# Kernel optimization log

Hardware: AMD Instinct MI355X
Metric: run time of the kernel (lower is better)

## Reference

```python
import jax, jax.numpy as jnp
import numpy as np

S = 20  # number of standard amino acids; hardcoded in the original layer


def expm_fixed(A, squarings=6, terms=14):
    """Scaling-and-squaring matrix exponential with fixed squaring count.
    A: (..., n, n). tau*Q entries are small (tau ~ softplus(-3)), so a fixed
    2^-6 scaling + Taylor-14 matches tf.linalg.expm to fp32 tolerance."""
    A = A / (2.0 ** squarings)
    I = jnp.broadcast_to(jnp.eye(A.shape[-1], dtype=A.dtype), A.shape)
    out = I
    term = I
    for i in range(1, terms + 1):
        term = jnp.matmul(term, A) / i
        out = out + term
    for _ in range(squarings):
        out = jnp.matmul(out, out)
    return out


def make_rate_matrix(R, p, eps=1e-16):
    """R: (N, s, s) symmetric exchangeabilities, zero diag. p: (N, s) equilibrium."""
    Q = R * p[:, None, :]                       # Q[i,j] = R[i,j] * p[j]
    diag = jnp.sum(Q, axis=-1, keepdims=True)   # (N, s, 1)
    eye = jnp.eye(Q.shape[-1], dtype=Q.dtype)
    Q = Q - diag * eye
    mue = jnp.sum(p[:, :, None] * diag, axis=-2, keepdims=True)  # (N,1,1)
    return Q / jnp.maximum(mue, eps)


def setup_inputs() -> dict:
    key = jax.random.key(0)
    ks = jax.random.split(key, 6)
    m, b, L, k, nr = 2, 256, 1024, 4, 100
    inputs = jax.random.uniform(ks[0], (m, b, L, S), dtype=jnp.float32)
    rate_indices = jax.random.randint(ks[1], (m, b), 0, nr, dtype=jnp.int64)
    # rate_init = constant(-3.0); small jitter so gradients are non-degenerate
    tau_kernel = -3.0 + 0.1 * jax.random.normal(ks[2], (m, nr), dtype=jnp.float32)
    exchangeability_kernel = 0.1 * jax.random.normal(ks[3], (m, k, S, S), dtype=jnp.float32)
    equilibrium_kernel = 0.1 * jax.random.normal(ks[4], (m, k, S), dtype=jnp.float32)
    per_matrix_rates_kernel = 0.1 * jax.random.normal(ks[5], (m, k), dtype=jnp.float32)
    return {
        "inputs": inputs,
        "tau_kernel": tau_kernel,
        "exchangeability_kernel": exchangeability_kernel,
        "equilibrium_kernel": equilibrium_kernel,
        "per_matrix_rates_kernel": per_matrix_rates_kernel,
        "rate_indices": rate_indices,
    }


def reference(inputs, tau_kernel, exchangeability_kernel, equilibrium_kernel,
              per_matrix_rates_kernel, rate_indices):
    m, b, L, s = inputs.shape
    k = exchangeability_kernel.shape[1]
    # make_tau(subset): gather per-sequence times then softplus
    tau = jax.nn.softplus(jnp.take_along_axis(tau_kernel, rate_indices, axis=1))  # (m,b)
    # per-matrix rates
    pmr = jax.nn.softplus(per_matrix_rates_kernel)  # (m,k)
    mut_rates = tau[:, :, None] * pmr[:, None, :]   # (m,b,k)
    # make_R: symmetrize, softplus, zero diagonal
    K = exchangeability_kernel
    R = jax.nn.softplus(0.5 * (K + jnp.swapaxes(K, -1, -2)))
    R = R * (1.0 - jnp.eye(s, dtype=R.dtype))       # (m,k,s,s)
    # make_p
    p = jax.nn.softmax(equilibrium_kernel, axis=-1)  # (m,k,s)
    # normalized rate matrices
    Q = make_rate_matrix(R.reshape(-1, s, s), p.reshape(-1, s)).reshape(m, k, s, s)
    # tau * Q, batched over sequences: (m,b,k,s,s)
    tauQ = mut_rates[..., None, None] * Q[:, None]
    P = expm_fixed(tauQ.reshape(-1, s, s)).reshape(m, b, k, s, s)
    # vector-format inputs path (non-transposed): mbLz,mbkzs->mbLks
    anc = jnp.einsum('mblz,mbkzs->mblks', inputs, P)
    # documented output: (num_model, b, L, num_matrices*s)
    return anc.reshape(m, b, L, k * s)
```

## Files before the change

kernel.cpp:

```cpp
#include <hip/hip_runtime.h>
#include <math.h>

#define M_  2
#define B_  256
#define L_  1024
#define K_  4
#define S_  20
#define NR_ 100
#define NTERM 7

typedef float f32x4_t __attribute__((ext_vector_type(4)));

__device__ __forceinline__ float softplusf(float x) {
    return x > 20.0f ? x : log1pf(expf(x));
}

__global__ __launch_bounds__(512)
void qpow_kernel(const float* __restrict__ exch,
                 const float* __restrict__ equil,
                 float*       __restrict__ Qpow)
{
    __shared__ float sQ[400];
    __shared__ float sT[2][400];
    __shared__ float sRow[20];

    const int blk = blockIdx.x;
    const int kk = blk % K_;
    const int mm = blk / K_;
    const int tid = threadIdx.x;
    const bool act = tid < 400;
    const int i = tid / 20;
    const int j = tid - i * 20;

    float p[20];
    float Q0 = 0.0f, rowsum = 0.0f;

    if (act) {
        const float* eq = equil + (mm * K_ + kk) * S_;
        float mx = eq[0];
        #pragma unroll
        for (int z = 1; z < 20; ++z) mx = fmaxf(mx, eq[z]);
        float s = 0.0f;
        #pragma unroll
        for (int z = 0; z < 20; ++z) { p[z] = expf(eq[z] - mx); s += p[z]; }
        const float inv = 1.0f / s;
        #pragma unroll
        for (int z = 0; z < 20; ++z) p[z] *= inv;

        const float* Kx = exch + (mm * K_ + kk) * S_ * S_;
        float R = (i == j) ? 0.0f : softplusf(0.5f * (Kx[i * 20 + j] + Kx[j * 20 + i]));
        Q0 = R * p[j];
        sQ[tid] = Q0;
    }
    __syncthreads();

    if (act) {
        rowsum = 0.0f;
        #pragma unroll
        for (int z = 0; z < 20; ++z) rowsum += sQ[i * 20 + z];
        if (j == 0) sRow[i] = rowsum;
    }
    __syncthreads();

    float* Tout = Qpow + (size_t)blk * (NTERM * 400);
    if (act) {
        float mue = 0.0f;
        #pragma unroll
        for (int z = 0; z < 20; ++z) mue += p[z] * sRow[z];
        float q = (Q0 - ((i == j) ? rowsum : 0.0f)) / fmaxf(mue, 1e-16f);
        sQ[tid] = q;
        sT[0][tid] = q;
        Tout[tid] = q;
    }
    __syncthreads();

    int cur = 0;
    for (int n = 2; n <= NTERM; ++n) {
        if (act) {
            float acc = 0.0f;
            #pragma unroll
            for (int z = 0; z < 20; ++z) acc += sT[cur][i * 20 + z] * sQ[z * 20 + j];
            acc /= (float)n;
            sT[cur ^ 1][tid] = acc;
            Tout[(n - 1) * 400 + tid] = acc;
        }
        __syncthreads();
        cur ^= 1;
    }
}

__global__ __launch_bounds__(512)
void pbuild_kernel(const float* __restrict__ Qpow,
                   const float* __restrict__ tauk,
                   const float* __restrict__ pmrk,
                   float*       __restrict__ Pws)
{
    const int blk = blockIdx.x;
    const int kk = blk % K_;
    const int rr = (blk / K_) % NR_;
    const int mm = blk / (K_ * NR_);
    const int tid = threadIdx.x;
    if (tid >= 400) return;

    const float mu = softplusf(tauk[mm * NR_ + rr]) * softplusf(pmrk[mm * K_ + kk]);
    const float* T = Qpow + ((size_t)(mm * K_ + kk) * NTERM) * 400 + tid;

    float acc = (tid % 21 == 0) ? 1.0f : 0.0f;
    float mp = mu;
    #pragma unroll
    for (int n = 0; n < NTERM; ++n) { acc = fmaf(mp, T[n * 400], acc); mp *= mu; }
    Pws[(size_t)blk * 400 + tid] = acc;
}

#define SPANR 256
#define TPB3  320

__device__ __forceinline__ void fma4(float4& a, float s, const float4& p) {
    a.x = fmaf(s, p.x, a.x);
    a.y = fmaf(s, p.y, a.y);
    a.z = fmaf(s, p.z, a.z);
    a.w = fmaf(s, p.w, a.w);
}

__device__ __forceinline__ void nt_store4(float* dst, const float4& v) {
    f32x4_t w;
    w.x = v.x; w.y = v.y; w.z = v.z; w.w = v.w;
    __builtin_nontemporal_store(w, (f32x4_t*)dst);
}

__global__ __launch_bounds__(TPB3)
void einsum_kernel(const float* __restrict__ inp,
                   const float* __restrict__ Pws,
                   const int*   __restrict__ ridx,
                   float*       __restrict__ out)
{
    __shared__ float Pl[K_ * 400];
    __shared__ float inL[SPANR * 20];

    const int bx      = blockIdx.x;
    const int quarter = bx & 3;
    const int mb      = bx >> 2;
    const int mm      = mb >> 8;
    const int tid     = threadIdx.x;
    const int t       = tid % 20;
    const int rg      = tid / 20;
    const int k       = t / 5;
    const int s0      = (t % 5) * 4;

    const int r = ridx[mb];

    {
        const float4* Psrc = (const float4*)(Pws + ((size_t)(mm * NR_ + r) * K_) * 400);
        float4* Pd = (float4*)Pl;
        Pd[tid] = Psrc[tid];
        if (tid < 80) Pd[320 + tid] = Psrc[320 + tid];

        const size_t row0g = (size_t)mb * L_ + (size_t)quarter * SPANR;
        const float4* Isrc = (const float4*)(inp + row0g * 20);
        float4* Id = (float4*)inL;
        #pragma unroll
        for (int q = 0; q < 4; ++q) Id[tid + q * TPB3] = Isrc[tid + q * TPB3];
    }
    __syncthreads();

    const size_t row0 = (size_t)mb * L_ + (size_t)quarter * SPANR;
    float* ob = out + row0 * 80 + k * 20 + s0;
    const float* Pk = Pl + k * 400 + s0;

    float4 acc[16];
    #pragma unroll
    for (int rr = 0; rr < 16; ++rr) acc[rr] = make_float4(0.f, 0.f, 0.f, 0.f);

    #pragma unroll
    for (int z4 = 0; z4 < 5; ++z4) {
        const float4 p0 = *(const float4*)(Pk + (z4 * 4 + 0) * 20);
        const float4 p1 = *(const float4*)(Pk + (z4 * 4 + 1) * 20);
        const float4 p2 = *(const float4*)(Pk + (z4 * 4 + 2) * 20);
        const float4 p3 = *(const float4*)(Pk + (z4 * 4 + 3) * 20);
        #pragma unroll
        for (int rr = 0; rr < 16; ++rr) {
            const int l = rg + rr * 16;
            const float4 av = *(const float4*)(inL + l * 20 + z4 * 4);
            fma4(acc[rr], av.x, p0);
            fma4(acc[rr], av.y, p1);
            fma4(acc[rr], av.z, p2);
            fma4(acc[rr], av.w, p3);
        }
    }

    #pragma unroll
    for (int rr = 0; rr < 16; ++rr) {
        const int l = rg + rr * 16;
        nt_store4(ob + (size_t)l * 80, acc[rr]);
    }
}

extern "C" void kernel_launch(void* const* d_in, const int* in_sizes, int n_in,
                              void* d_out, int out_size, void* d_ws, size_t ws_size,
                              hipStream_t stream) {
    const float* inp   = (const float*)d_in[0];
    const float* tauk  = (const float*)d_in[1];
    const float* exch  = (const float*)d_in[2];
    const float* equil = (const float*)d_in[3];
    const float* pmrk  = (const float*)d_in[4];
    const int*   ridx  = (const int*)d_in[5];
    float* outp = (float*)d_out;

    float* Qpow = (float*)d_ws;
    float* Pws  = Qpow + (size_t)M_ * K_ * NTERM * 400;

    qpow_kernel<<<M_ * K_, 512, 0, stream>>>(exch, equil, Qpow);
    pbuild_kernel<<<M_ * NR_ * K_, 512, 0, stream>>>(Qpow, tauk, pmrk, Pws);
    einsum_kernel<<<M_ * B_ * (L_ / SPANR), TPB3, 0, stream>>>(inp, Pws, ridx, outp);
}
```

Before: 57.69 us.

## Fuse Q-power and P-build kernels; use plain stores in einsum

Merges the Taylor-term kernel and the per-rate P builder into one kernel. Each thread keeps its seven Q-power terms in registers and loops over all 100 rates to write P directly, which removes one launch and the workspace round trip. The trade-off is that the P build now runs on only 8 blocks instead of 800, so this stage loses parallelism. The einsum output also switches from nontemporal stores to ordinary float4 stores.

```diff
diff --git a/kernel.cpp b/kernel.cpp
--- a/kernel.cpp
+++ b/kernel.cpp
@@ -9,16 +9,16 @@
 #define NR_ 100
 #define NTERM 7
 
-typedef float f32x4_t __attribute__((ext_vector_type(4)));
-
 __device__ __forceinline__ float softplusf(float x) {
     return x > 20.0f ? x : log1pf(expf(x));
 }
 
 __global__ __launch_bounds__(512)
-void qpow_kernel(const float* __restrict__ exch,
+void pmat_kernel(const float* __restrict__ tauk,
+                 const float* __restrict__ exch,
                  const float* __restrict__ equil,
-                 float*       __restrict__ Qpow)
+                 const float* __restrict__ pmrk,
+                 float*       __restrict__ Pws)
 {
     __shared__ float sQ[400];
     __shared__ float sT[2][400];
@@ -34,6 +34,7 @@
 
     float p[20];
     float Q0 = 0.0f, rowsum = 0.0f;
+    float tn[NTERM];
 
     if (act) {
         const float* eq = equil + (mm * K_ + kk) * S_;
@@ -62,7 +63,6 @@
     }
     __syncthreads();
 
-    float* Tout = Qpow + (size_t)blk * (NTERM * 400);
     if (act) {
         float mue = 0.0f;
         #pragma unroll
@@ -70,7 +70,7 @@
         float q = (Q0 - ((i == j) ? rowsum : 0.0f)) / fmaxf(mue, 1e-16f);
         sQ[tid] = q;
         sT[0][tid] = q;
-        Tout[tid] = q;
+        tn[0] = q;
     }
     __syncthreads();
 
@@ -81,35 +81,25 @@
             #pragma unroll
             for (int z = 0; z < 20; ++z) acc += sT[cur][i * 20 + z] * sQ[z * 20 + j];
             acc /= (float)n;
+            tn[n - 1] = acc;
             sT[cur ^ 1][tid] = acc;
-            Tout[(n - 1) * 400 + tid] = acc;
         }
         __syncthreads();
         cur ^= 1;
     }
-}
 
-__global__ __launch_bounds__(512)
-void pbuild_kernel(const float* __restrict__ Qpow,
-                   const float* __restrict__ tauk,
-                   const float* __restrict__ pmrk,
-                   float*       __restrict__ Pws)
-{
-    const int blk = blockIdx.x;
-    const int kk = blk % K_;
-    const int rr = (blk / K_) % NR_;
-    const int mm = blk / (K_ * NR_);
-    const int tid = threadIdx.x;
-    if (tid >= 400) return;
-
-    const float mu = softplusf(tauk[mm * NR_ + rr]) * softplusf(pmrk[mm * K_ + kk]);
-    const float* T = Qpow + ((size_t)(mm * K_ + kk) * NTERM) * 400 + tid;
-
-    float acc = (tid % 21 == 0) ? 1.0f : 0.0f;
-    float mp = mu;
-    #pragma unroll
-    for (int n = 0; n < NTERM; ++n) { acc = fmaf(mp, T[n * 400], acc); mp *= mu; }
-    Pws[(size_t)blk * 400 + tid] = acc;
+    if (act) {
+        const float pm = softplusf(pmrk[mm * K_ + kk]);
+        const float idn = (i == j) ? 1.0f : 0.0f;
+        for (int rr = 0; rr < NR_; ++rr) {
+            const float mu = softplusf(tauk[mm * NR_ + rr]) * pm;
+            float a = idn;
+            float mp = mu;
+            #pragma unroll
+            for (int n = 0; n < NTERM; ++n) { a = fmaf(mp, tn[n], a); mp *= mu; }
+            Pws[((size_t)(mm * NR_ + rr) * K_ + kk) * 400 + tid] = a;
+        }
+    }
 }
 
 #define SPANR 256
@@ -120,12 +110,6 @@
     a.y = fmaf(s, p.y, a.y);
     a.z = fmaf(s, p.z, a.z);
     a.w = fmaf(s, p.w, a.w);
-}
-
-__device__ __forceinline__ void nt_store4(float* dst, const float4& v) {
-    f32x4_t w;
-    w.x = v.x; w.y = v.y; w.z = v.z; w.w = v.w;
-    __builtin_nontemporal_store(w, (f32x4_t*)dst);
 }
 
 __global__ __launch_bounds__(TPB3)
@@ -191,7 +175,7 @@
     #pragma unroll
     for (int rr = 0; rr < 16; ++rr) {
         const int l = rg + rr * 16;
-        nt_store4(ob + (size_t)l * 80, acc[rr]);
+        *(float4*)(ob + (size_t)l * 80) = acc[rr];
     }
 }
 
@@ -206,10 +190,8 @@
     const int*   ridx  = (const int*)d_in[5];
     float* outp = (float*)d_out;
 
-    float* Qpow = (float*)d_ws;
-    float* Pws  = Qpow + (size_t)M_ * K_ * NTERM * 400;
+    float* Pws = (float*)d_ws;
 
-    qpow_kernel<<<M_ * K_, 512, 0, stream>>>(exch, equil, Qpow);
-    pbuild_kernel<<<M_ * NR_ * K_, 512, 0, stream>>>(Qpow, tauk, pmrk, Pws);
+    pmat_kernel<<<M_ * K_, 512, 0, stream>>>(tauk, exch, equil, pmrk, Pws);
     einsum_kernel<<<M_ * B_ * (L_ / SPANR), TPB3, 0, stream>>>(inp, Pws, ridx, outp);
 }
```

Result: slower. 103.6 us (+79.6%).
